# Performance work log

Hardware: AMD Instinct MI355X
Metric: run time of the kernel (lower is better)

The kernel has to match this reference:

```python
import jax, jax.numpy as jnp
import numpy as np

NUM_EXPERTS = 32
TOP_K = 4
ALPHA = 1.702   # GPT-OSS GLU alpha
LIMIT = 7.0     # GPT-OSS clamp limit


def setup_inputs() -> dict:
    key = jax.random.key(0)
    ks = jax.random.split(key, 7)
    B, S, H, E = 2, 2048, 1024, NUM_EXPERTS
    return {
        "hidden_states": jax.random.normal(ks[0], (B, S, H), jnp.float32),
        "router_weight": jax.random.normal(ks[1], (E, H), jnp.float32) * 0.02,
        "router_bias": jax.random.normal(ks[2], (E,), jnp.float32) * 0.02,
        "gate_up_proj": jax.random.normal(ks[3], (E, H, 2 * H), jnp.float32) * 0.02,
        "gate_up_proj_bias": jax.random.normal(ks[4], (E, 2 * H), jnp.float32) * 0.02,
        "down_proj": jax.random.normal(ks[5], (E, H, H), jnp.float32) * 0.02,
        "down_proj_bias": jax.random.normal(ks[6], (E, H), jnp.float32) * 0.02,
    }


def _moe_forward(hidden_states, router_weight, router_bias,
                 gate_up_proj, gate_up_proj_bias, down_proj, down_proj_bias):
    B, S, H = hidden_states.shape
    E, K = NUM_EXPERTS, TOP_K
    T = B * S
    capacity = T * K // E * 2  # expert_capacity as in the torch module

    x = hidden_states.reshape(T, H)

    # ---- router: linear -> top-k -> softmax over top-k -> dense scatter ----
    logits = x @ router_weight.T + router_bias                     # [T, E]
    top_vals, top_idx = jax.lax.top_k(logits, K)                   # [T, K]
    weights = jax.nn.softmax(top_vals, axis=-1)                    # [T, K]
    router_scores = jnp.zeros_like(logits).at[
        jnp.arange(T)[:, None], top_idx].set(weights)              # [T, E]

    # ---- capacity-based dispatch (first-come-first-served in token order) ----
    flat_e = top_idx.reshape(-1)                                   # [T*K]
    token_id = jnp.repeat(jnp.arange(T), K)                        # [T*K]
    onehot = (flat_e[:, None] == jnp.arange(E)[None, :]).astype(jnp.int32)
    # rank of each assignment within its expert (0-based, arrival order)
    rank = jnp.take_along_axis(jnp.cumsum(onehot, axis=0),
                               flat_e[:, None], axis=1)[:, 0] - 1  # [T*K]
    valid = rank < capacity
    slot = jnp.where(valid, rank, capacity)  # out-of-range slot -> dropped

    buffer = jnp.zeros((E, capacity, H), x.dtype).at[flat_e, slot].set(
        x[token_id], mode="drop")                                  # [E, C, H]

    # ---- grouped expert MLP: gate_up GEMM + GPT-OSS GLU + down GEMM ----
    gu = jnp.einsum("ech,ehf->ecf", buffer, gate_up_proj) \
         + gate_up_proj_bias[:, None, :]                           # [E, C, 2H]
    gate = gu[..., ::2]
    up = gu[..., 1::2]
    gate = jnp.minimum(gate, LIMIT)
    up = jnp.clip(up, -LIMIT, LIMIT)
    glu = gate * jax.nn.sigmoid(gate * ALPHA)
    act = (up + 1.0) * glu                                         # [E, C, H]
    expert_out = jnp.einsum("ech,ehf->ecf", act, down_proj) \
                 + down_proj_bias[:, None, :]                      # [E, C, H]

    # ---- weighted combine (dropped tokens contribute zero) ----
    gathered = expert_out[flat_e, jnp.where(valid, rank, 0)]       # [T*K, H]
    w = router_scores[token_id, flat_e] * valid.astype(x.dtype)    # [T*K]
    out = jax.ops.segment_sum(gathered * w[:, None], token_id,
                              num_segments=T)                      # [T, H]
    return out.reshape(B, S, H), router_scores


def reference(hidden_states, router_weight, router_bias, gate_up_proj,
              gate_up_proj_bias, down_proj, down_proj_bias):
    return _moe_forward(hidden_states, router_weight, router_bias,
                        gate_up_proj, gate_up_proj_bias, down_proj,
                        down_proj_bias)
```

## Files before the change

kernel.cpp:

```cpp
#include <hip/hip_runtime.h>
#include <hip/hip_bf16.h>

#define T_TOK 4096
#define H_DIM 1024
#define E_EXP 32
#define TOPK 4
#define CAP 1024
#define PAIRS (T_TOK*TOPK)

typedef __attribute__((ext_vector_type(8))) short short8v;
typedef __attribute__((ext_vector_type(4))) short short4v;
typedef __attribute__((ext_vector_type(4))) float f32x4;
typedef unsigned long long u64;

__device__ __forceinline__ unsigned bf16r(float f) {
    unsigned u = __float_as_uint(f);
    return ((u + 0x7fffu + ((u >> 16) & 1u)) >> 16) & 0xffffu;
}
__device__ __forceinline__ u64 pack4bf(float a, float b, float c, float d) {
    return (u64)(bf16r(a) | (bf16r(b) << 16)) |
           ((u64)(bf16r(c) | (bf16r(d) << 16)) << 32);
}

__global__ void zero_kernel(float4* __restrict__ p, int n4) {
    int i = blockIdx.x * blockDim.x + threadIdx.x;
    if (i < n4) p[i] = make_float4(0.f, 0.f, 0.f, 0.f);
}

__global__ __launch_bounds__(256) void router_kernel(
    const float* __restrict__ x,
    const float* __restrict__ rw,
    const float* __restrict__ rb,
    float* __restrict__ scores,
    int* __restrict__ flat_e,
    float* __restrict__ flat_w)
{
    __shared__ float xs[H_DIM];
    __shared__ float lg[E_EXP];
    __shared__ float sw[TOPK];
    __shared__ int   se[TOPK];
    const int t = blockIdx.x;
    const int tid = threadIdx.x;

    for (int i = tid; i < H_DIM; i += 256) xs[i] = x[(size_t)t * H_DIM + i];
    __syncthreads();

    const int e = tid >> 3;
    const int l8 = tid & 7;
    float partial = 0.f;
    const float* wr = rw + (size_t)e * H_DIM;
    for (int h = l8; h < H_DIM; h += 8) partial += xs[h] * wr[h];
    partial += __shfl_xor(partial, 1);
    partial += __shfl_xor(partial, 2);
    partial += __shfl_xor(partial, 4);
    if (l8 == 0) lg[e] = partial + rb[e];
    __syncthreads();

    if (tid == 0) {
        unsigned used = 0;
        float bv[TOPK]; int bi[TOPK];
        #pragma unroll
        for (int j = 0; j < TOPK; j++) {
            float best = -1e30f; int bid = -1;
            for (int q = 0; q < E_EXP; q++) {
                if (used & (1u << q)) continue;
                if (lg[q] > best) { best = lg[q]; bid = q; }
            }
            used |= 1u << bid;
            bv[j] = best; bi[j] = bid;
        }
        const float m = bv[0];
        float s = 0.f; float w[TOPK];
        #pragma unroll
        for (int j = 0; j < TOPK; j++) { w[j] = expf(bv[j] - m); s += w[j]; }
        const float inv = 1.f / s;
        #pragma unroll
        for (int j = 0; j < TOPK; j++) { sw[j] = w[j] * inv; se[j] = bi[j]; }
    }
    __syncthreads();

    if (tid < E_EXP) {
        float v = 0.f;
        #pragma unroll
        for (int j = 0; j < TOPK; j++) if (se[j] == tid) v = sw[j];
        scores[(size_t)t * E_EXP + tid] = v;
    }
    if (tid < TOPK) {
        flat_e[t * TOPK + tid] = se[tid];
        flat_w[t * TOPK + tid] = sw[tid];
    }
}

__global__ __launch_bounds__(256) void scan_kernel(
    const int* __restrict__ flat_e, const float* __restrict__ flat_w,
    int* __restrict__ slot_token, float* __restrict__ slot_w,
    int* __restrict__ counts)
{
    __shared__ int cnt[256 * E_EXP];
    const int tid = threadIdx.x;
    for (int e = 0; e < E_EXP; e++) cnt[tid * E_EXP + e] = 0;
    __syncthreads();
    const int base = tid * (PAIRS / 256);
    for (int i = 0; i < PAIRS / 256; i++) {
        int e = flat_e[base + i];
        cnt[tid * E_EXP + e]++;
    }
    __syncthreads();
    if (tid < E_EXP) {
        int run = 0;
        for (int i = 0; i < 256; i++) {
            int idx = i * E_EXP + tid;
            int v = cnt[idx];
            cnt[idx] = run;
            run += v;
        }
        counts[tid] = min(run, CAP);
    }
    __syncthreads();
    for (int i = 0; i < PAIRS / 256; i++) {
        int p = base + i;
        int e = flat_e[p];
        int r = cnt[tid * E_EXP + e]++;
        if (r < CAP) {
            slot_token[e * CAP + r] = p >> 2;
            slot_w[e * CAP + r] = flat_w[p];
        }
    }
}

__global__ __launch_bounds__(256, 2) void gateup_mfma(
    const float* __restrict__ x,
    const float* __restrict__ wgu,
    const float* __restrict__ gub,
    const int* __restrict__ slot_token,
    const int* __restrict__ counts,
    short* __restrict__ act)
{
    const int lin = blockIdx.x;
    const int xcd = lin & 7, slot = lin >> 3;
    const int gg = (slot >> 3) * 8 + xcd;
    const int rt = slot & 7;
    const int e = gg >> 4, ct = gg & 15;

    const int n = counts[e];
    const int row0 = rt * 128;
    if (row0 >= n) return;
    const int rows_here = min(128, n - row0);
    const int c0f = ct * 64;
    const int c0gu = ct * 128;

    __shared__ short As[128 * 32];
    __shared__ short Bg[8 * 64 * 4];
    __shared__ short Bu[8 * 64 * 4];
    __shared__ int tok_s[128];

    const int tid = threadIdx.x;
    if (tid < 128)
        tok_s[tid] = (tid < rows_here) ? slot_token[e * CAP + row0 + tid] : -1;
    __syncthreads();

    const int lane = tid & 63, wid = tid >> 6;
    const int wr = wid >> 1, wc = wid & 1;
    const int l15 = lane & 15, l4 = lane >> 4;

    f32x4 accg[4][2], accu[4][2];
    #pragma unroll
    for (int m = 0; m < 4; m++)
        #pragma unroll
        for (int j = 0; j < 2; j++) { accg[m][j] = (f32x4)0.f; accu[m][j] = (f32x4)0.f; }

    float4 av[4];
    float2 bgv[2][4];

    auto prefetch = [&](int k0) {
        #pragma unroll
        for (int i = 0; i < 4; ++i) {
            int lin2 = tid + 256 * i;
            int r = lin2 >> 3, kq = lin2 & 7;
            int tk = tok_s[r];
            av[i] = (tk >= 0) ? *(const float4*)(x + (size_t)tk * H_DIM + k0 + kq * 4)
                              : make_float4(0.f, 0.f, 0.f, 0.f);
        }
        #pragma unroll
        for (int u = 0; u < 2; ++u) {
            int lin2 = tid + 256 * u;
            int f = lin2 & 63, kq = lin2 >> 6;
            const float* src = wgu + ((size_t)e * H_DIM + k0 + kq * 4) * 2048 + c0gu + 2 * f;
            #pragma unroll
            for (int q = 0; q < 4; ++q) bgv[u][q] = *(const float2*)(src + (size_t)q * 2048);
        }
    };
    auto stage = [&]() {
        #pragma unroll
        for (int i = 0; i < 4; ++i) {
            int lin2 = tid + 256 * i;
            int r = lin2 >> 3, kq = lin2 & 7;
            int dst = (r * 64 + kq * 8) ^ ((r & 3) << 4);
            *(u64*)((char*)As + dst) = pack4bf(av[i].x, av[i].y, av[i].z, av[i].w);
        }
        #pragma unroll
        for (int u = 0; u < 2; ++u) {
            int lin2 = tid + 256 * u;
            int f = lin2 & 63, kq = lin2 >> 6;
            *(u64*)((char*)Bg + kq * 512 + f * 8) =
                pack4bf(bgv[u][0].x, bgv[u][1].x, bgv[u][2].x, bgv[u][3].x);
            *(u64*)((char*)Bu + kq * 512 + f * 8) =
                pack4bf(bgv[u][0].y, bgv[u][1].y, bgv[u][2].y, bgv[u][3].y);
        }
    };

    prefetch(0);
    for (int t = 0; t < 32; ++t) {
        if (t) __syncthreads();
        stage();
        __syncthreads();
        if (t < 31) prefetch((t + 1) * 32);

        short8v afr[4];
        #pragma unroll
        for (int m = 0; m < 4; ++m) {
            int row = wr * 64 + m * 16 + l15;
            int off = (row * 64 + l4 * 16) ^ ((row & 3) << 4);
            afr[m] = *(short8v*)((char*)As + off);
        }
        #pragma unroll
        for (int j = 0; j < 2; ++j) {
            int f = wc * 32 + j * 16 + l15;
            short4v glo = *(short4v*)((char*)Bg + (2 * l4) * 512 + f * 8);
            short4v ghi = *(short4v*)((char*)Bg + (2 * l4 + 1) * 512 + f * 8);
            short4v ulo = *(short4v*)((char*)Bu + (2 * l4) * 512 + f * 8);
            short4v uhi = *(short4v*)((char*)Bu + (2 * l4 + 1) * 512 + f * 8);
            short8v bg8 = __builtin_shufflevector(glo, ghi, 0, 1, 2, 3, 4, 5, 6, 7);
            short8v bu8 = __builtin_shufflevector(ulo, uhi, 0, 1, 2, 3, 4, 5, 6, 7);
            #pragma unroll
            for (int m = 0; m < 4; ++m) {
                accg[m][j] = __builtin_amdgcn_mfma_f32_16x16x32_bf16(afr[m], bg8, accg[m][j], 0, 0, 0);
                accu[m][j] = __builtin_amdgcn_mfma_f32_16x16x32_bf16(afr[m], bu8, accu[m][j], 0, 0, 0);
            }
        }
    }

    #pragma unroll
    for (int j = 0; j < 2; ++j) {
        int f = c0f + wc * 32 + j * 16 + l15;
        float bgb = gub[(size_t)e * 2048 + 2 * f];
        float bub = gub[(size_t)e * 2048 + 2 * f + 1];
        #pragma unroll
        for (int m = 0; m < 4; ++m) {
            int rbase = wr * 64 + m * 16 + l4 * 4;
            #pragma unroll
            for (int reg = 0; reg < 4; ++reg) {
                int r = rbase + reg;
                if (r >= rows_here) continue;
                float g = accg[m][j][reg] + bgb;
                float u = accu[m][j][reg] + bub;
                g = fminf(g, 7.0f);
                u = fminf(fmaxf(u, -7.0f), 7.0f);
                float glu = g / (1.0f + __expf(-1.702f * g));
                float a = (u + 1.0f) * glu;
                act[((size_t)e * CAP + row0 + r) * H_DIM + f] = (short)bf16r(a);
            }
        }
    }
}

__global__ __launch_bounds__(256, 2) void down_mfma(
    const short* __restrict__ act,
    const float* __restrict__ wd,
    const float* __restrict__ db,
    const int* __restrict__ slot_token,
    const float* __restrict__ slot_w,
    const int* __restrict__ counts,
    float* __restrict__ out)
{
    const int lin = blockIdx.x;
    const int xcd = lin & 7, slot = lin >> 3;
    const int gg = (slot >> 3) * 8 + xcd;
    const int rt = slot & 7;
    const int e = gg >> 3, ct = gg & 7;

    const int n = counts[e];
    const int row0 = rt * 128;
    if (row0 >= n) return;
    const int rows_here = min(128, n - row0);
    const int c0 = ct * 128;

    __shared__ short As[128 * 32];
    __shared__ short Bs[8 * 128 * 4];
    __shared__ int tok_s[128];
    __shared__ float wrow_s[128];

    const int tid = threadIdx.x;
    if (tid < 128) {
        if (tid < rows_here) {
            tok_s[tid] = slot_token[e * CAP + row0 + tid];
            wrow_s[tid] = slot_w[e * CAP + row0 + tid];
        } else { tok_s[tid] = 0; wrow_s[tid] = 0.f; }
    }
    __syncthreads();

    const int lane = tid & 63, wid = tid >> 6;
    const int wr = wid >> 1, wc = wid & 1;
    const int l15 = lane & 15, l4 = lane >> 4;

    f32x4 acc[4][4];
    #pragma unroll
    for (int m = 0; m < 4; m++)
        #pragma unroll
        for (int j = 0; j < 4; j++) acc[m][j] = (f32x4)0.f;

    uint4 avd[2];
    float2 bvd[2][4];

    auto prefetch = [&](int k0) {
        #pragma unroll
        for (int i = 0; i < 2; ++i) {
            int lin2 = tid + 256 * i;
            int r = lin2 >> 2, o = lin2 & 3;
            avd[i] = (r < rows_here)
                ? *(const uint4*)(act + ((size_t)e * CAP + row0 + r) * H_DIM + k0 + o * 8)
                : make_uint4(0, 0, 0, 0);
        }
        #pragma unroll
        for (int u = 0; u < 2; ++u) {
            int lin2 = tid + 256 * u;
            int np = lin2 & 63, kq = lin2 >> 6;
            const float* src = wd + ((size_t)e * H_DIM + k0 + kq * 4) * H_DIM + c0 + 2 * np;
            #pragma unroll
            for (int q = 0; q < 4; ++q) bvd[u][q] = *(const float2*)(src + (size_t)q * H_DIM);
        }
    };
    auto stage = [&]() {
        #pragma unroll
        for (int i = 0; i < 2; ++i) {
            int lin2 = tid + 256 * i;
            int r = lin2 >> 2, o = lin2 & 3;
            int dst = (r * 64 + o * 16) ^ ((r & 3) << 4);
            *(uint4*)((char*)As + dst) = avd[i];
        }
        #pragma unroll
        for (int u = 0; u < 2; ++u) {
            int lin2 = tid + 256 * u;
            int np = lin2 & 63, kq = lin2 >> 6;
            int n0 = 2 * np;
            *(u64*)((char*)Bs + kq * 1024 + n0 * 8) =
                pack4bf(bvd[u][0].x, bvd[u][1].x, bvd[u][2].x, bvd[u][3].x);
            *(u64*)((char*)Bs + kq * 1024 + n0 * 8 + 8) =
                pack4bf(bvd[u][0].y, bvd[u][1].y, bvd[u][2].y, bvd[u][3].y);
        }
    };

    prefetch(0);
    for (int t = 0; t < 32; ++t) {
        if (t) __syncthreads();
        stage();
        __syncthreads();
        if (t < 31) prefetch((t + 1) * 32);

        short8v afr[4];
        #pragma unroll
        for (int m = 0; m < 4; ++m) {
            int row = wr * 64 + m * 16 + l15;
            int off = (row * 64 + l4 * 16) ^ ((row & 3) << 4);
            afr[m] = *(short8v*)((char*)As + off);
        }
        #pragma unroll
        for (int j = 0; j < 4; ++j) {
            int nn = wc * 64 + j * 16 + l15;
            short4v lo = *(short4v*)((char*)Bs + (2 * l4) * 1024 + nn * 8);
            short4v hi = *(short4v*)((char*)Bs + (2 * l4 + 1) * 1024 + nn * 8);
            short8v b8 = __builtin_shufflevector(lo, hi, 0, 1, 2, 3, 4, 5, 6, 7);
            #pragma unroll
            for (int m = 0; m < 4; ++m)
                acc[m][j] = __builtin_amdgcn_mfma_f32_16x16x32_bf16(afr[m], b8, acc[m][j], 0, 0, 0);
        }
    }

    #pragma unroll
    for (int j = 0; j < 4; ++j) {
        int col = c0 + wc * 64 + j * 16 + l15;
        float bias = db[(size_t)e * H_DIM + col];
        #pragma unroll
        for (int m = 0; m < 4; ++m) {
            int rbase = wr * 64 + m * 16 + l4 * 4;
            #pragma unroll
            for (int reg = 0; reg < 4; ++reg) {
                int r = rbase + reg;
                if (r >= rows_here) continue;
                atomicAdd(out + (size_t)tok_s[r] * H_DIM + col,
                          wrow_s[r] * (acc[m][j][reg] + bias));
            }
        }
    }
}

extern "C" void kernel_launch(void* const* d_in, const int* in_sizes, int n_in,
                              void* d_out, int out_size, void* d_ws, size_t ws_size,
                              hipStream_t stream) {
    const float* x   = (const float*)d_in[0];
    const float* rw  = (const float*)d_in[1];
    const float* rb  = (const float*)d_in[2];
    const float* wgu = (const float*)d_in[3];
    const float* gub = (const float*)d_in[4];
    const float* wd  = (const float*)d_in[5];
    const float* db  = (const float*)d_in[6];

    float* out    = (float*)d_out;
    float* scores = out + (size_t)T_TOK * H_DIM;

    char* ws = (char*)d_ws;
    short* act = (short*)ws;
    size_t off = (size_t)E_EXP * CAP * H_DIM * 2;
    int*   flat_e     = (int*)(ws + off);   off += PAIRS * 4;
    float* flat_w     = (float*)(ws + off); off += PAIRS * 4;
    int*   slot_token = (int*)(ws + off);   off += E_EXP * CAP * 4;
    float* slot_w     = (float*)(ws + off); off += E_EXP * CAP * 4;
    int*   counts     = (int*)(ws + off);   off += E_EXP * 4;
    (void)ws_size; (void)out_size; (void)n_in; (void)in_sizes;

    hipLaunchKernelGGL(zero_kernel, dim3(4096), dim3(256), 0, stream,
                       (float4*)out, (T_TOK * H_DIM) / 4);
    hipLaunchKernelGGL(router_kernel, dim3(T_TOK), dim3(256), 0, stream,
                       x, rw, rb, scores, flat_e, flat_w);
    hipLaunchKernelGGL(scan_kernel, dim3(1), dim3(256), 0, stream,
                       flat_e, flat_w, slot_token, slot_w, counts);
    hipLaunchKernelGGL(gateup_mfma, dim3(4096), dim3(256), 0, stream,
                       x, wgu, gub, slot_token, counts, act);
    hipLaunchKernelGGL(down_mfma, dim3(2048), dim3(256), 0, stream,
                       act, wd, db, slot_token, slot_w, counts, out);
}
```

Baseline: 502.6 us.

## Pre-stage bf16 token tiles, double-buffer MFMA loops, replace atomics with gather combine

A new kernel gathers the dispatched tokens once, converts them to bf16 and stores them in a pre-swizzled tile layout. The gate/up and down GEMMs then load their A tiles straight into LDS with global_load_lds and run a double-buffered loop with one barrier per k-step. The conversions use the packed v_cvt_pk_bf16_f32 instruction, and occupancy hints rise to 3 blocks per SM. The down kernel now writes bf16 expert outputs instead of doing fp32 atomics, and a finalize kernel gathers each token's top-k rows with their weights, which removes the zeroing kernel and atomic contention. The cost is extra workspace traffic, two more launches, and bf16 rounding of expert outputs before the combine.

```diff
diff --git a/kernel.cpp b/kernel.cpp
--- a/kernel.cpp
+++ b/kernel.cpp
@@ -12,28 +12,33 @@
 typedef __attribute__((ext_vector_type(4))) short short4v;
 typedef __attribute__((ext_vector_type(4))) float f32x4;
 typedef unsigned long long u64;
-
+typedef unsigned short ushort;
+
+__device__ __forceinline__ float bf16_bits_to_f32(ushort h) {
+    return __uint_as_float(((unsigned)h) << 16);
+}
 __device__ __forceinline__ unsigned bf16r(float f) {
     unsigned u = __float_as_uint(f);
     return ((u + 0x7fffu + ((u >> 16) & 1u)) >> 16) & 0xffffu;
 }
-__device__ __forceinline__ u64 pack4bf(float a, float b, float c, float d) {
-    return (u64)(bf16r(a) | (bf16r(b) << 16)) |
-           ((u64)(bf16r(c) | (bf16r(d) << 16)) << 32);
-}
-
-__global__ void zero_kernel(float4* __restrict__ p, int n4) {
-    int i = blockIdx.x * blockDim.x + threadIdx.x;
-    if (i < n4) p[i] = make_float4(0.f, 0.f, 0.f, 0.f);
-}
+__device__ __forceinline__ unsigned cvt2(float a, float b) {
+    unsigned r;
+    asm("v_cvt_pk_bf16_f32 %0, %1, %2" : "=v"(r) : "v"(a), "v"(b));
+    return r;
+}
+__device__ __forceinline__ u64 pk4(float a, float b, float c, float d) {
+    return (u64)cvt2(a, b) | ((u64)cvt2(c, d) << 32);
+}
+
+#define GLD16(gsrc, ldst) \
+    __builtin_amdgcn_global_load_lds( \
+        (const __attribute__((address_space(1))) unsigned*)(gsrc), \
+        (__attribute__((address_space(3))) unsigned*)(ldst), 16, 0, 0)
 
 __global__ __launch_bounds__(256) void router_kernel(
-    const float* __restrict__ x,
-    const float* __restrict__ rw,
-    const float* __restrict__ rb,
-    float* __restrict__ scores,
-    int* __restrict__ flat_e,
-    float* __restrict__ flat_w)
+    const float* __restrict__ x, const float* __restrict__ rw,
+    const float* __restrict__ rb, float* __restrict__ scores,
+    int* __restrict__ flat_e, float* __restrict__ flat_w)
 {
     __shared__ float xs[H_DIM];
     __shared__ float lg[E_EXP];
@@ -45,8 +50,7 @@
     for (int i = tid; i < H_DIM; i += 256) xs[i] = x[(size_t)t * H_DIM + i];
     __syncthreads();
 
-    const int e = tid >> 3;
-    const int l8 = tid & 7;
+    const int e = tid >> 3, l8 = tid & 7;
     float partial = 0.f;
     const float* wr = rw + (size_t)e * H_DIM;
     for (int h = l8; h < H_DIM; h += 8) partial += xs[h] * wr[h];
@@ -94,7 +98,7 @@
 __global__ __launch_bounds__(256) void scan_kernel(
     const int* __restrict__ flat_e, const float* __restrict__ flat_w,
     int* __restrict__ slot_token, float* __restrict__ slot_w,
-    int* __restrict__ counts)
+    int* __restrict__ pair_slot, int* __restrict__ counts)
 {
     __shared__ int cnt[256 * E_EXP];
     const int tid = threadIdx.x;
@@ -124,17 +128,47 @@
         if (r < CAP) {
             slot_token[e * CAP + r] = p >> 2;
             slot_w[e * CAP + r] = flat_w[p];
-        }
-    }
-}
-
-__global__ __launch_bounds__(256, 2) void gateup_mfma(
-    const float* __restrict__ x,
+            pair_slot[p] = r;
+        } else {
+            pair_slot[p] = -1;
+        }
+    }
+}
+
+__global__ __launch_bounds__(256) void stage_tokens(
+    const float* __restrict__ x, const int* __restrict__ slot_token,
+    const int* __restrict__ counts, char* __restrict__ xbuf)
+{
+    const int e = blockIdx.y, rt = blockIdx.x;
+    const int n = counts[e];
+    const int row0 = rt * 128;
+    if (row0 >= n) return;
+    const int rows_here = min(128, n - row0);
+    const int lane = threadIdx.x & 63, wv = threadIdx.x >> 6;
+    char* tb = xbuf + ((size_t)(e * 8 + rt)) * 262144;
+
+    for (int r = wv; r < rows_here; r += 4) {
+        const float* xr = x + (size_t)slot_token[e * CAP + row0 + r] * H_DIM;
+        #pragma unroll
+        for (int q = 0; q < 2; ++q) {
+            int g = q * 64 + lane;
+            float4 a = *(const float4*)(xr + g * 8);
+            float4 b = *(const float4*)(xr + g * 8 + 4);
+            uint4 w;
+            w.x = cvt2(a.x, a.y); w.y = cvt2(a.z, a.w);
+            w.z = cvt2(b.x, b.y); w.w = cvt2(b.z, b.w);
+            int kb = g >> 2, gi = g & 3;
+            *(uint4*)(tb + kb * 8192 + r * 64 + ((gi ^ (r & 3)) * 16)) = w;
+        }
+    }
+}
+
+__global__ __launch_bounds__(256, 3) void gateup_mfma(
+    const char* __restrict__ xbuf,
     const float* __restrict__ wgu,
     const float* __restrict__ gub,
-    const int* __restrict__ slot_token,
     const int* __restrict__ counts,
-    short* __restrict__ act)
+    char* __restrict__ act)
 {
     const int lin = blockIdx.x;
     const int xcd = lin & 7, slot = lin >> 3;
@@ -146,90 +180,77 @@
     const int row0 = rt * 128;
     if (row0 >= n) return;
     const int rows_here = min(128, n - row0);
-    const int c0f = ct * 64;
-    const int c0gu = ct * 128;
-
-    __shared__ short As[128 * 32];
-    __shared__ short Bg[8 * 64 * 4];
-    __shared__ short Bu[8 * 64 * 4];
-    __shared__ int tok_s[128];
+    const int c0f = ct * 64, c0gu = ct * 128;
+
+    __shared__ char AsB[2][8192];
+    __shared__ char BgB[2][4096];
+    __shared__ char BuB[2][4096];
 
     const int tid = threadIdx.x;
-    if (tid < 128)
-        tok_s[tid] = (tid < rows_here) ? slot_token[e * CAP + row0 + tid] : -1;
-    __syncthreads();
-
     const int lane = tid & 63, wid = tid >> 6;
     const int wr = wid >> 1, wc = wid & 1;
     const int l15 = lane & 15, l4 = lane >> 4;
 
+    const char* xtile = xbuf + ((size_t)(e * 8 + rt)) * 262144;
+
     f32x4 accg[4][2], accu[4][2];
     #pragma unroll
     for (int m = 0; m < 4; m++)
         #pragma unroll
         for (int j = 0; j < 2; j++) { accg[m][j] = (f32x4)0.f; accu[m][j] = (f32x4)0.f; }
 
-    float4 av[4];
     float2 bgv[2][4];
-
-    auto prefetch = [&](int k0) {
-        #pragma unroll
-        for (int i = 0; i < 4; ++i) {
-            int lin2 = tid + 256 * i;
-            int r = lin2 >> 3, kq = lin2 & 7;
-            int tk = tok_s[r];
-            av[i] = (tk >= 0) ? *(const float4*)(x + (size_t)tk * H_DIM + k0 + kq * 4)
-                              : make_float4(0.f, 0.f, 0.f, 0.f);
-        }
+    const int bnp = tid & 63;
+    const int bkq0 = tid >> 6;
+
+    auto stageA = [&](int buf, int t) {
+        const char* src = xtile + (size_t)t * 8192 + wid * 2048 + lane * 16;
+        char* dst = AsB[buf] + wid * 2048;
+        GLD16(src, dst);
+        GLD16(src + 1024, dst + 1024);
+    };
+    auto bload = [&](int k0) {
         #pragma unroll
         for (int u = 0; u < 2; ++u) {
-            int lin2 = tid + 256 * u;
-            int f = lin2 & 63, kq = lin2 >> 6;
-            const float* src = wgu + ((size_t)e * H_DIM + k0 + kq * 4) * 2048 + c0gu + 2 * f;
+            int kq = bkq0 + 4 * u;
+            const float* src = wgu + ((size_t)e * H_DIM + k0 + kq * 4) * 2048 + c0gu + 2 * bnp;
             #pragma unroll
             for (int q = 0; q < 4; ++q) bgv[u][q] = *(const float2*)(src + (size_t)q * 2048);
         }
     };
-    auto stage = [&]() {
-        #pragma unroll
-        for (int i = 0; i < 4; ++i) {
-            int lin2 = tid + 256 * i;
-            int r = lin2 >> 3, kq = lin2 & 7;
-            int dst = (r * 64 + kq * 8) ^ ((r & 3) << 4);
-            *(u64*)((char*)As + dst) = pack4bf(av[i].x, av[i].y, av[i].z, av[i].w);
-        }
+    auto bpack = [&](int buf) {
         #pragma unroll
         for (int u = 0; u < 2; ++u) {
-            int lin2 = tid + 256 * u;
-            int f = lin2 & 63, kq = lin2 >> 6;
-            *(u64*)((char*)Bg + kq * 512 + f * 8) =
-                pack4bf(bgv[u][0].x, bgv[u][1].x, bgv[u][2].x, bgv[u][3].x);
-            *(u64*)((char*)Bu + kq * 512 + f * 8) =
-                pack4bf(bgv[u][0].y, bgv[u][1].y, bgv[u][2].y, bgv[u][3].y);
-        }
-    };
-
-    prefetch(0);
+            int kq = bkq0 + 4 * u;
+            *(u64*)(BgB[buf] + kq * 512 + bnp * 8) =
+                pk4(bgv[u][0].x, bgv[u][1].x, bgv[u][2].x, bgv[u][3].x);
+            *(u64*)(BuB[buf] + kq * 512 + bnp * 8) =
+                pk4(bgv[u][0].y, bgv[u][1].y, bgv[u][2].y, bgv[u][3].y);
+        }
+    };
+
+    bload(0);
+    stageA(0, 0);
+    bpack(0);
+    __syncthreads();
+    int cur = 0;
+
     for (int t = 0; t < 32; ++t) {
-        if (t) __syncthreads();
-        stage();
-        __syncthreads();
-        if (t < 31) prefetch((t + 1) * 32);
+        if (t < 31) { bload((t + 1) * 32); stageA(cur ^ 1, t + 1); }
 
         short8v afr[4];
         #pragma unroll
         for (int m = 0; m < 4; ++m) {
             int row = wr * 64 + m * 16 + l15;
-            int off = (row * 64 + l4 * 16) ^ ((row & 3) << 4);
-            afr[m] = *(short8v*)((char*)As + off);
+            afr[m] = *(short8v*)(AsB[cur] + row * 64 + ((l4 ^ (row & 3)) * 16));
         }
         #pragma unroll
         for (int j = 0; j < 2; ++j) {
             int f = wc * 32 + j * 16 + l15;
-            short4v glo = *(short4v*)((char*)Bg + (2 * l4) * 512 + f * 8);
-            short4v ghi = *(short4v*)((char*)Bg + (2 * l4 + 1) * 512 + f * 8);
-            short4v ulo = *(short4v*)((char*)Bu + (2 * l4) * 512 + f * 8);
-            short4v uhi = *(short4v*)((char*)Bu + (2 * l4 + 1) * 512 + f * 8);
+            short4v glo = *(short4v*)(BgB[cur] + (2 * l4) * 512 + f * 8);
+            short4v ghi = *(short4v*)(BgB[cur] + (2 * l4 + 1) * 512 + f * 8);
+            short4v ulo = *(short4v*)(BuB[cur] + (2 * l4) * 512 + f * 8);
+            short4v uhi = *(short4v*)(BuB[cur] + (2 * l4 + 1) * 512 + f * 8);
             short8v bg8 = __builtin_shufflevector(glo, ghi, 0, 1, 2, 3, 4, 5, 6, 7);
             short8v bu8 = __builtin_shufflevector(ulo, uhi, 0, 1, 2, 3, 4, 5, 6, 7);
             #pragma unroll
@@ -238,13 +259,18 @@
                 accu[m][j] = __builtin_amdgcn_mfma_f32_16x16x32_bf16(afr[m], bu8, accu[m][j], 0, 0, 0);
             }
         }
-    }
-
+        if (t < 31) bpack(cur ^ 1);
+        __syncthreads();
+        cur ^= 1;
+    }
+
+    char* atile = act + ((size_t)(e * 8 + rt)) * 262144;
     #pragma unroll
     for (int j = 0; j < 2; ++j) {
         int f = c0f + wc * 32 + j * 16 + l15;
         float bgb = gub[(size_t)e * 2048 + 2 * f];
         float bub = gub[(size_t)e * 2048 + 2 * f + 1];
+        int kb = f >> 5, gi = (f & 31) >> 3, ke = f & 7;
         #pragma unroll
         for (int m = 0; m < 4; ++m) {
             int rbase = wr * 64 + m * 16 + l4 * 4;
@@ -258,20 +284,19 @@
                 u = fminf(fmaxf(u, -7.0f), 7.0f);
                 float glu = g / (1.0f + __expf(-1.702f * g));
                 float a = (u + 1.0f) * glu;
-                act[((size_t)e * CAP + row0 + r) * H_DIM + f] = (short)bf16r(a);
+                *(ushort*)(atile + kb * 8192 + r * 64 + ((gi ^ (r & 3)) * 16) + ke * 2)
+                    = (ushort)bf16r(a);
             }
         }
     }
 }
 
-__global__ __launch_bounds__(256, 2) void down_mfma(
-    const short* __restrict__ act,
+__global__ __launch_bounds__(256, 3) void down_mfma(
+    const char* __restrict__ act,
     const float* __restrict__ wd,
     const float* __restrict__ db,
-    const int* __restrict__ slot_token,
-    const float* __restrict__ slot_w,
     const int* __restrict__ counts,
-    float* __restrict__ out)
+    ushort* __restrict__ eout)
 {
     const int lin = blockIdx.x;
     const int xcd = lin & 7, slot = lin >> 3;
@@ -285,95 +310,79 @@
     const int rows_here = min(128, n - row0);
     const int c0 = ct * 128;
 
-    __shared__ short As[128 * 32];
-    __shared__ short Bs[8 * 128 * 4];
-    __shared__ int tok_s[128];
-    __shared__ float wrow_s[128];
+    __shared__ char AsB[2][8192];
+    __shared__ char BsB[2][8192];
 
     const int tid = threadIdx.x;
-    if (tid < 128) {
-        if (tid < rows_here) {
-            tok_s[tid] = slot_token[e * CAP + row0 + tid];
-            wrow_s[tid] = slot_w[e * CAP + row0 + tid];
-        } else { tok_s[tid] = 0; wrow_s[tid] = 0.f; }
-    }
-    __syncthreads();
-
     const int lane = tid & 63, wid = tid >> 6;
     const int wr = wid >> 1, wc = wid & 1;
     const int l15 = lane & 15, l4 = lane >> 4;
 
+    const char* atile = act + ((size_t)(e * 8 + rt)) * 262144;
+
     f32x4 acc[4][4];
     #pragma unroll
     for (int m = 0; m < 4; m++)
         #pragma unroll
         for (int j = 0; j < 4; j++) acc[m][j] = (f32x4)0.f;
 
-    uint4 avd[2];
     float2 bvd[2][4];
-
-    auto prefetch = [&](int k0) {
-        #pragma unroll
-        for (int i = 0; i < 2; ++i) {
-            int lin2 = tid + 256 * i;
-            int r = lin2 >> 2, o = lin2 & 3;
-            avd[i] = (r < rows_here)
-                ? *(const uint4*)(act + ((size_t)e * CAP + row0 + r) * H_DIM + k0 + o * 8)
-                : make_uint4(0, 0, 0, 0);
-        }
+    const int bnp = tid & 63;
+    const int bkq0 = tid >> 6;
+
+    auto stageA = [&](int buf, int t) {
+        const char* src = atile + (size_t)t * 8192 + wid * 2048 + lane * 16;
+        char* dst = AsB[buf] + wid * 2048;
+        GLD16(src, dst);
+        GLD16(src + 1024, dst + 1024);
+    };
+    auto bload = [&](int k0) {
         #pragma unroll
         for (int u = 0; u < 2; ++u) {
-            int lin2 = tid + 256 * u;
-            int np = lin2 & 63, kq = lin2 >> 6;
-            const float* src = wd + ((size_t)e * H_DIM + k0 + kq * 4) * H_DIM + c0 + 2 * np;
+            int kq = bkq0 + 4 * u;
+            const float* src = wd + ((size_t)e * H_DIM + k0 + kq * 4) * H_DIM + c0 + 2 * bnp;
             #pragma unroll
             for (int q = 0; q < 4; ++q) bvd[u][q] = *(const float2*)(src + (size_t)q * H_DIM);
         }
     };
-    auto stage = [&]() {
-        #pragma unroll
-        for (int i = 0; i < 2; ++i) {
-            int lin2 = tid + 256 * i;
-            int r = lin2 >> 2, o = lin2 & 3;
-            int dst = (r * 64 + o * 16) ^ ((r & 3) << 4);
-            *(uint4*)((char*)As + dst) = avd[i];
-        }
+    auto bpack = [&](int buf) {
         #pragma unroll
         for (int u = 0; u < 2; ++u) {
-            int lin2 = tid + 256 * u;
-            int np = lin2 & 63, kq = lin2 >> 6;
-            int n0 = 2 * np;
-            *(u64*)((char*)Bs + kq * 1024 + n0 * 8) =
-                pack4bf(bvd[u][0].x, bvd[u][1].x, bvd[u][2].x, bvd[u][3].x);
-            *(u64*)((char*)Bs + kq * 1024 + n0 * 8 + 8) =
-                pack4bf(bvd[u][0].y, bvd[u][1].y, bvd[u][2].y, bvd[u][3].y);
-        }
-    };
-
-    prefetch(0);
+            int kq = bkq0 + 4 * u;
+            char* dst = BsB[buf] + kq * 1024 + bnp * 16;
+            *(u64*)dst       = pk4(bvd[u][0].x, bvd[u][1].x, bvd[u][2].x, bvd[u][3].x);
+            *(u64*)(dst + 8) = pk4(bvd[u][0].y, bvd[u][1].y, bvd[u][2].y, bvd[u][3].y);
+        }
+    };
+
+    bload(0);
+    stageA(0, 0);
+    bpack(0);
+    __syncthreads();
+    int cur = 0;
+
     for (int t = 0; t < 32; ++t) {
-        if (t) __syncthreads();
-        stage();
-        __syncthreads();
-        if (t < 31) prefetch((t + 1) * 32);
+        if (t < 31) { bload((t + 1) * 32); stageA(cur ^ 1, t + 1); }
 
         short8v afr[4];
         #pragma unroll
         for (int m = 0; m < 4; ++m) {
             int row = wr * 64 + m * 16 + l15;
-            int off = (row * 64 + l4 * 16) ^ ((row & 3) << 4);
-            afr[m] = *(short8v*)((char*)As + off);
+            afr[m] = *(short8v*)(AsB[cur] + row * 64 + ((l4 ^ (row & 3)) * 16));
         }
         #pragma unroll
         for (int j = 0; j < 4; ++j) {
             int nn = wc * 64 + j * 16 + l15;
-            short4v lo = *(short4v*)((char*)Bs + (2 * l4) * 1024 + nn * 8);
-            short4v hi = *(short4v*)((char*)Bs + (2 * l4 + 1) * 1024 + nn * 8);
+            short4v lo = *(short4v*)(BsB[cur] + (2 * l4) * 1024 + nn * 8);
+            short4v hi = *(short4v*)(BsB[cur] + (2 * l4 + 1) * 1024 + nn * 8);
             short8v b8 = __builtin_shufflevector(lo, hi, 0, 1, 2, 3, 4, 5, 6, 7);
             #pragma unroll
             for (int m = 0; m < 4; ++m)
                 acc[m][j] = __builtin_amdgcn_mfma_f32_16x16x32_bf16(afr[m], b8, acc[m][j], 0, 0, 0);
         }
+        if (t < 31) bpack(cur ^ 1);
+        __syncthreads();
+        cur ^= 1;
     }
 
     #pragma unroll
@@ -387,11 +396,36 @@
             for (int reg = 0; reg < 4; ++reg) {
                 int r = rbase + reg;
                 if (r >= rows_here) continue;
-                atomicAdd(out + (size_t)tok_s[r] * H_DIM + col,
-                          wrow_s[r] * (acc[m][j][reg] + bias));
+                eout[((size_t)e * CAP + row0 + r) * H_DIM + col] =
+                    (ushort)bf16r(acc[m][j][reg] + bias);
             }
         }
     }
+}
+
+__global__ __launch_bounds__(256) void finalize_kernel(
+    const ushort* __restrict__ eout, const int* __restrict__ flat_e,
+    const float* __restrict__ flat_w, const int* __restrict__ pair_slot,
+    float* __restrict__ out)
+{
+    const int t = blockIdx.x;
+    const int c = threadIdx.x * 4;
+    float a0 = 0.f, a1 = 0.f, a2 = 0.f, a3 = 0.f;
+    #pragma unroll
+    for (int k = 0; k < TOPK; ++k) {
+        int p = t * TOPK + k;
+        int s = pair_slot[p];
+        if (s < 0) continue;
+        int e = flat_e[p];
+        float w = flat_w[p];
+        const ushort* row = eout + ((size_t)e * CAP + s) * H_DIM + c;
+        ushort4 v = *(const ushort4*)row;
+        a0 += w * bf16_bits_to_f32(v.x);
+        a1 += w * bf16_bits_to_f32(v.y);
+        a2 += w * bf16_bits_to_f32(v.z);
+        a3 += w * bf16_bits_to_f32(v.w);
+    }
+    *(float4*)(out + (size_t)t * H_DIM + c) = make_float4(a0, a1, a2, a3);
 }
 
 extern "C" void kernel_launch(void* const* d_in, const int* in_sizes, int n_in,
@@ -409,23 +443,28 @@
     float* scores = out + (size_t)T_TOK * H_DIM;
 
     char* ws = (char*)d_ws;
-    short* act = (short*)ws;
+    char* xbuf = ws;
+    ushort* eout = (ushort*)ws;
     size_t off = (size_t)E_EXP * CAP * H_DIM * 2;
+    char* act = ws + off;          off += (size_t)E_EXP * CAP * H_DIM * 2;
     int*   flat_e     = (int*)(ws + off);   off += PAIRS * 4;
     float* flat_w     = (float*)(ws + off); off += PAIRS * 4;
     int*   slot_token = (int*)(ws + off);   off += E_EXP * CAP * 4;
     float* slot_w     = (float*)(ws + off); off += E_EXP * CAP * 4;
+    int*   pair_slot  = (int*)(ws + off);   off += PAIRS * 4;
     int*   counts     = (int*)(ws + off);   off += E_EXP * 4;
-    (void)ws_size; (void)out_size; (void)n_in; (void)in_sizes;
-
-    hipLaunchKernelGGL(zero_kernel, dim3(4096), dim3(256), 0, stream,
-                       (float4*)out, (T_TOK * H_DIM) / 4);
+    (void)ws_size; (void)out_size; (void)n_in; (void)in_sizes; (void)slot_w;
+
     hipLaunchKernelGGL(router_kernel, dim3(T_TOK), dim3(256), 0, stream,
                        x, rw, rb, scores, flat_e, flat_w);
     hipLaunchKernelGGL(scan_kernel, dim3(1), dim3(256), 0, stream,
-                       flat_e, flat_w, slot_token, slot_w, counts);
+                       flat_e, flat_w, slot_token, slot_w, pair_slot, counts);
+    hipLaunchKernelGGL(stage_tokens, dim3(8, E_EXP), dim3(256), 0, stream,
+                       x, slot_token, counts, xbuf);
     hipLaunchKernelGGL(gateup_mfma, dim3(4096), dim3(256), 0, stream,
-                       x, wgu, gub, slot_token, counts, act);
+                       xbuf, wgu, gub, counts, act);
     hipLaunchKernelGGL(down_mfma, dim3(2048), dim3(256), 0, stream,
-                       act, wd, db, slot_token, slot_w, counts, out);
-}
+                       act, wd, db, counts, eout);
+    hipLaunchKernelGGL(finalize_kernel, dim3(T_TOK), dim3(256), 0, stream,
+                       eout, flat_e, flat_w, pair_slot, out);
+}
```

Result: no change. 494.4 us (-1.6%).
